# Kernel tuning notes

Measured on AMD Instinct MI355X. Metric: run time of the kernel, lower is better.

## Reference

```python
import jax, jax.numpy as jnp
import numpy as np

N_NODES = 50000
N_EDGES = 800000
F_IN = 2
T = 12
HID = 64
OUT = 12
K = 2  # diffusion order: identity + 1-hop (out- and in-directed)


def setup_inputs() -> dict:
    key = jax.random.key(0)
    ks = jax.random.split(key, 12)
    inp = {}
    inp["x"] = jax.random.normal(ks[0], (1, N_NODES, F_IN, T), dtype=jnp.float32)
    inp["edge_index"] = jax.random.randint(ks[1], (2, N_EDGES), 0, N_NODES)
    inp["edge_weight"] = jax.random.uniform(ks[2], (N_EDGES,), dtype=jnp.float32)

    def u(k, shape, fan):
        s = 1.0 / np.sqrt(fan)
        return jax.random.uniform(k, shape, jnp.float32, -s, s)

    c1 = F_IN + HID   # 66: DCRNN gates operate on cat([X, H])
    c2 = HID + HID    # 128
    inp["w1z"] = u(ks[3], (2, K, c1, HID), c1); inp["b1z"] = jnp.zeros((HID,), jnp.float32)
    inp["w1r"] = u(ks[4], (2, K, c1, HID), c1); inp["b1r"] = jnp.zeros((HID,), jnp.float32)
    inp["w1h"] = u(ks[5], (2, K, c1, HID), c1); inp["b1h"] = jnp.zeros((HID,), jnp.float32)
    inp["w2z"] = u(ks[6], (2, K, c2, HID), c2); inp["b2z"] = jnp.zeros((HID,), jnp.float32)
    inp["w2r"] = u(ks[7], (2, K, c2, HID), c2); inp["b2r"] = jnp.zeros((HID,), jnp.float32)
    inp["w2h"] = u(ks[8], (2, K, c2, HID), c2); inp["b2h"] = jnp.zeros((HID,), jnp.float32)
    inp["lin_w"] = u(ks[9], (HID, OUT), HID)
    inp["lin_b"] = u(ks[10], (OUT,), HID)
    return inp


def _dconv(X, row, col, norm_out, norm_in, w, b):
    # K=2 diffusion conv: H = X@W[:,0] + (D_O^-1 W diffusion)@W[0,1] + (D_I^-1 W^T diffusion)@W[1,1] + b
    H = X @ w[0, 0] + X @ w[1, 0]
    Xr = X[row]  # gather source-node features per edge: [E, C]
    Tx_o = jax.ops.segment_sum(norm_out[:, None] * Xr, col, num_segments=N_NODES)
    Tx_i = jax.ops.segment_sum(norm_in[:, None] * Xr, col, num_segments=N_NODES)
    return H + Tx_o @ w[0, 1] + Tx_i @ w[1, 1] + b


def _cell(X, H, row, col, no, ni, wz, bz, wr, br, wh, bh):
    # GRU-style DCRNN cell
    XH = jnp.concatenate([X, H], axis=1)
    Z = jax.nn.sigmoid(_dconv(XH, row, col, no, ni, wz, bz))
    R = jax.nn.sigmoid(_dconv(XH, row, col, no, ni, wr, br))
    Ht = jnp.tanh(_dconv(jnp.concatenate([X, R * H], axis=1), row, col, no, ni, wh, bh))
    return Z * H + (1.0 - Z) * Ht


def reference(x, edge_index, edge_weight, w1z, b1z, w1r, b1r, w1h, b1h,
              w2z, b2z, w2r, b2r, w2h, b2h, lin_w, lin_b):
    row, col = edge_index[0], edge_index[1]
    deg_out = jax.ops.segment_sum(edge_weight, row, num_segments=N_NODES)
    deg_in = jax.ops.segment_sum(edge_weight, col, num_segments=N_NODES)
    norm_out = edge_weight / deg_out[row]  # per-edge weight of D_O^{-1} W
    norm_in = edge_weight / deg_in[col]    # per-edge weight of D_I^{-1} W^T
    xs = jnp.transpose(x[0], (2, 0, 1))    # [T, N, F] (batch = 1)

    def step(carry, xt):
        h1, h2 = carry
        h1 = jax.nn.relu(_cell(xt, h1, row, col, norm_out, norm_in, w1z, b1z, w1r, b1r, w1h, b1h))
        h2 = jax.nn.relu(_cell(h1, h2, row, col, norm_out, norm_in, w2z, b2z, w2r, b2r, w2h, b2h))
        return (h1, h2), None

    h0 = jnp.zeros((N_NODES, HID), x.dtype)
    (h1, h2), _ = jax.lax.scan(step, (h0, h0), xs)
    out = h2 @ lin_w + lin_b  # [N, 12]
    return out.reshape(1, N_NODES, OUT)
```

## Files before the change

### kernel.cpp

```cpp
#include <hip/hip_runtime.h>

#define NN 50000
#define NE 800000
#define TT 12
#define NBIN (4 * NN)
#define NBLK ((NBIN + 255) / 256)

typedef _Float16 h16;
typedef __attribute__((ext_vector_type(2))) _Float16 h16x2;
typedef __attribute__((ext_vector_type(4))) _Float16 h16x4;
typedef __attribute__((ext_vector_type(8))) _Float16 half8;
typedef __attribute__((ext_vector_type(4))) float f32x4;
typedef __attribute__((address_space(3))) h16 as3h16;
typedef __attribute__((address_space(3))) half8 as3half8;

static constexpr size_t alignup(size_t x) { return (x + 255) & ~(size_t)255; }
static constexpr size_t O_CNT  = 0;
static constexpr size_t O_CUR  = alignup(O_CNT + NBIN + 1);
static constexpr size_t O_DEGO = alignup(O_CUR + NBIN);
static constexpr size_t O_BSUM = alignup(O_DEGO + NN);
static constexpr size_t O_BEXC = O_BSUM + 1024;
static constexpr size_t O_EDG  = alignup(O_BEXC + 1024);
static constexpr size_t O_TXX  = alignup(O_EDG + (size_t)NE * 2);
static constexpr size_t O_WF1ZR= alignup(O_TXX + (size_t)TT * NN * 4);
static constexpr size_t O_WF1H = alignup(O_WF1ZR + 12288);
static constexpr size_t O_WF2ZR= alignup(O_WF1H + 6144);
static constexpr size_t O_WF2H = alignup(O_WF2ZR + 24576);
static constexpr size_t O_WX1ZR= alignup(O_WF2H + 12288);
static constexpr size_t O_WX1H = alignup(O_WX1ZR + 768);
static constexpr size_t O_PX0  = alignup(O_WX1H + 384);
static constexpr size_t O_PX1  = O_PX0 + (size_t)NN * 64;
static constexpr size_t O_PZR  = O_PX1 + (size_t)NN * 64;
static constexpr size_t O_Z1   = O_PZR + (size_t)NN * 64;
static constexpr size_t O_Z2   = O_Z1 + (size_t)NN * 32;
static constexpr size_t O_TXA  = alignup(O_Z2 + (size_t)NN * 32);
static constexpr size_t O_TXB  = alignup(O_TXA + (size_t)NN * 64);
static constexpr size_t WS_FLOATS = O_TXB + (size_t)NN * 128;

__device__ __forceinline__ float sigm_(float x) { return 1.f / (1.f + __expf(-x)); }
__device__ __forceinline__ float tanh_(float x) { float e = __expf(2.f * x); return 1.f - 2.f / (e + 1.f); }

__device__ __forceinline__ void gld_lds16(const h16* g, as3h16* l) {
    __builtin_amdgcn_global_load_lds(
        (const __attribute__((address_space(1))) void*)g,
        (__attribute__((address_space(3))) void*)l, 16, 0, 0);
}

template <int N>
__device__ __forceinline__ void wait_lgkm0_vm() {
    if constexpr (N == 0)      asm volatile("s_waitcnt lgkmcnt(0) vmcnt(0)" ::: "memory");
    else if constexpr (N == 1) asm volatile("s_waitcnt lgkmcnt(0) vmcnt(1)" ::: "memory");
    else                       asm volatile("s_waitcnt lgkmcnt(0) vmcnt(2)" ::: "memory");
}


__global__ __launch_bounds__(256) void k_zero(float* ws) {
    size_t i = (size_t)blockIdx.x * 256 + threadIdx.x;
    size_t stride = (size_t)gridDim.x * 256;
    for (size_t p = i; p < O_BSUM + 2048; p += stride) ((int*)ws)[p] = 0;
    for (size_t p = i; p < (size_t)NN * 128; p += stride) ws[O_PX0 + p] = 0.f;
    for (size_t p = i; p < (size_t)NN * 128; p += stride) ws[O_TXB + p] = 0.f;
}

__global__ __launch_bounds__(256) void k_hist(const int* ei, float* ws) {
    int e = blockIdx.x * 256 + threadIdx.x;
    if (e >= NE) return;
    int r = ei[e], c = ei[NE + e];
    int bin = c * 4 + r / 12500;
    int rk = atomicAdd((int*)ws + O_CNT + bin, 1);
    ((int*)ws)[O_TXX + e] = rk;
}

__global__ __launch_bounds__(256) void k_scanA(float* ws) {
    __shared__ int sh[256];
    int t = threadIdx.x, i = blockIdx.x * 256 + t;
    int v = (i < NBIN) ? ((int*)ws)[O_CNT + i] : 0;
    sh[t] = v; __syncthreads();
    for (int o = 128; o > 0; o >>= 1) { if (t < o) sh[t] += sh[t + o]; __syncthreads(); }
    if (t == 0) ((int*)ws)[O_BSUM + blockIdx.x] = sh[0];
}

__global__ __launch_bounds__(256) void k_scanB(float* ws) {
    __shared__ int tot[256];
    int t = threadIdx.x;
    int* bsum = (int*)ws + O_BSUM;
    int* bexc = (int*)ws + O_BEXC;
    int base = t * 4;
    int v0 = (base + 0 < NBLK) ? bsum[base + 0] : 0;
    int v1 = (base + 1 < NBLK) ? bsum[base + 1] : 0;
    int v2 = (base + 2 < NBLK) ? bsum[base + 2] : 0;
    int v3 = (base + 3 < NBLK) ? bsum[base + 3] : 0;
    int sum = v0 + v1 + v2 + v3;
    tot[t] = sum; __syncthreads();
    for (int o = 1; o < 256; o <<= 1) {
        int a = (t >= o) ? tot[t - o] : 0;
        __syncthreads(); tot[t] += a; __syncthreads();
    }
    int excl = tot[t] - sum;
    if (base + 0 < NBLK) bexc[base + 0] = excl;
    if (base + 1 < NBLK) bexc[base + 1] = excl + v0;
    if (base + 2 < NBLK) bexc[base + 2] = excl + v0 + v1;
    if (base + 3 < NBLK) bexc[base + 3] = excl + v0 + v1 + v2;
    if (t == 255) ((int*)ws)[O_CNT + NBIN] = tot[255];
}

__global__ __launch_bounds__(256) void k_scanC(float* ws) {
    __shared__ int sh[256];
    int t = threadIdx.x, b = blockIdx.x, i = b * 256 + t;
    int v = (i < NBIN) ? ((int*)ws)[O_CNT + i] : 0;
    sh[t] = v; __syncthreads();
    for (int o = 1; o < 256; o <<= 1) {
        int a = (t >= o) ? sh[t - o] : 0;
        __syncthreads(); sh[t] += a; __syncthreads();
    }
    if (i < NBIN) ((int*)ws)[O_CNT + i] = ((int*)ws)[O_BEXC + b] + sh[t] - v;
}

__global__ __launch_bounds__(256) void k_scatter(const int* ei, const float* ew, float* ws) {
    int e = blockIdx.x * 256 + threadIdx.x;
    if (e >= NE) return;
    int r = ei[e], c = ei[NE + e];
    float w = ew[e];
    atomicAdd(ws + O_DEGO + r, w);
    int bin = c * 4 + r / 12500;
    int p = ((const int*)ws)[O_CNT + bin] + ((const int*)ws)[O_TXX + e];
    uint2 rec; rec.x = (unsigned)r; rec.y = __float_as_uint(w);
    ((uint2*)(ws + O_EDG))[p] = rec;
}

__global__ __launch_bounds__(256) void k_norm(float* ws) {
    int n = blockIdx.x * 4 + (threadIdx.x >> 6);
    int lane = threadIdx.x & 63;
    const int* offs = (const int*)ws + O_CNT;
    uint2* recs = (uint2*)(ws + O_EDG);
    const float* dego = ws + O_DEGO;
    int e0 = offs[4 * n], e1 = offs[4 * n + 4];
    float s = 0.f;
    for (int e = e0 + lane; e < e1; e += 64) s += __uint_as_float(recs[e].y);
    #pragma unroll
    for (int m = 1; m < 64; m <<= 1) s += __shfl_xor(s, m);
    float inv = 1.f / s;
    for (int e = e0 + lane; e < e1; e += 64) {
        uint2 r = recs[e];
        float w = __uint_as_float(r.y);
        h16x2 nv; nv.x = (h16)(w / dego[r.x]); nv.y = (h16)(w * inv);
        r.y = __builtin_bit_cast(unsigned int, nv);
        recs[e] = r;
    }
}

__global__ __launch_bounds__(256) void k_aggx(const float* __restrict__ x, float* __restrict__ ws) {
    int tid = threadIdx.x;
    int n = blockIdx.x * 8 + (tid >> 5);
    int l = tid & 31;
    const int* offs = (const int*)ws + O_CNT;
    const uint2* recs = (const uint2*)(ws + O_EDG);
    int e0 = offs[4 * n], e1 = offs[4 * n + 4];
    int f = l / 12, tt2 = l % 12;
    bool act = l < 24;
    float ao = 0.f, ai = 0.f;
    uint2 rc0, rc1;
    if (e0 < e1) {
        rc0 = recs[e0];
        rc1 = recs[(e0 + 1 < e1) ? e0 + 1 : e1 - 1];
    }
    for (int e = e0; e < e1; e += 2) {
        uint2 c0 = rc0, c1 = rc1;
        int n2 = (e + 2 < e1) ? e + 2 : e1 - 1, n3 = (e + 3 < e1) ? e + 3 : e1 - 1;
        rc0 = recs[n2]; rc1 = recs[n3];
        h16x2 nv0 = __builtin_bit_cast(h16x2, c0.y);
        h16x2 nv1 = __builtin_bit_cast(h16x2, c1.y);
        bool ok1 = (e + 1 < e1);
        float no1 = ok1 ? (float)nv1.x : 0.f, ni1 = ok1 ? (float)nv1.y : 0.f;
        if (act) {
            float v0 = x[(size_t)c0.x * 24 + f * 12 + tt2];
            float v1 = x[(size_t)c1.x * 24 + f * 12 + tt2];
            ao += (float)nv0.x * v0 + no1 * v1;
            ai += (float)nv0.y * v0 + ni1 * v1;
        }
    }
    if (act) {
        ws[O_TXX + ((size_t)tt2 * NN + n) * 4 + f] = ao;
        ws[O_TXX + ((size_t)tt2 * NN + n) * 4 + 2 + f] = ai;
    }
}

__device__ void packf_dev(int L, int NO, const float* wa, const float* wb, h16* Wf, int idx) {
    int C = (L == 1) ? 66 : 128;
    int NT = NO / 16;
    int j = idx & 7, l = (idx >> 3) & 63;
    int rest = idx >> 9;
    int ct = rest % NT, ks = rest / NT;
    int k = ks * 32 + ((l >> 4) << 3) + j;
    int col = ct * 16 + (l & 15);
    const float* w = wa; int jj = col;
    if (NO == 128 && col >= 64) { w = wb; jj = col - 64; }
    int G = k >> 6, c6 = k & 63, sg, crow;
    if (L == 1) { sg = G; crow = 2 + c6; }
    else        { sg = G >> 1; crow = ((G & 1) << 6) + c6; }
    float v;
    if (sg == 0)      v = w[(size_t)(0 * C + crow) * 64 + jj] + w[(size_t)(2 * C + crow) * 64 + jj];
    else if (sg == 1) v = w[(size_t)(1 * C + crow) * 64 + jj];
    else              v = w[(size_t)(3 * C + crow) * 64 + jj];
    Wf[idx] = (h16)v;
}

__device__ void packx_dev(int NO, const float* wa, const float* wb, float* Wx, int idx) {
    if (idx >= 6 * NO) return;
    int cc = idx / NO, col = idx % NO;
    const float* w = wa; int jj = col;
    if (NO == 128 && col >= 64) { w = wb; jj = col - 64; }
    int sg = cc >> 1, c = cc & 1;
    float v;
    if (sg == 0)      v = w[(size_t)(0 * 66 + c) * 64 + jj] + w[(size_t)(2 * 66 + c) * 64 + jj];
    else if (sg == 1) v = w[(size_t)(1 * 66 + c) * 64 + jj];
    else              v = w[(size_t)(3 * 66 + c) * 64 + jj];
    Wx[idx] = v;
}

__global__ __launch_bounds__(256) void k_packall(const float* w1z, const float* w1r, const float* w1h,
    const float* w2z, const float* w2r, const float* w2h, float* ws) {
    int b = blockIdx.x, t = threadIdx.x;
    if (b < 96)       packf_dev(1, 128, w1z, w1r, (h16*)(ws + O_WF1ZR), b * 256 + t);
    else if (b < 144) packf_dev(1, 64,  w1h, nullptr, (h16*)(ws + O_WF1H), (b - 96) * 256 + t);
    else if (b < 336) packf_dev(2, 128, w2z, w2r, (h16*)(ws + O_WF2ZR), (b - 144) * 256 + t);
    else if (b < 432) packf_dev(2, 64,  w2h, nullptr, (h16*)(ws + O_WF2H), (b - 336) * 256 + t);
    else {
        int idx = (b - 432) * 256 + t;
        if (idx < 768) packx_dev(128, w1z, w1r, ws + O_WX1ZR, idx);
        int idx2 = idx - 768;
        if (idx2 >= 0 && idx2 < 384) packx_dev(64, w1h, nullptr, ws + O_WX1H, idx2);
    }
}

__global__ __launch_bounds__(256) void k_aggP(
    const h16* __restrict__ T,
    h16* __restrict__ outA, int orsA, int oA, int iA,
    h16* __restrict__ outB, int orsB, int oB, int iB,
    const float* __restrict__ ws) {
    int tid = threadIdx.x, lane = tid & 63, wv = tid >> 6;
    int q = lane >> 4, fl = lane & 15;
    int n = blockIdx.x * 16 + wv * 4 + q;
    const int* offs = (const int*)ws + O_CNT;
    const uint2* recs = (const uint2*)(ws + O_EDG);
    int e0 = offs[4 * n], e1 = offs[4 * n + 4];
    float ao[8] = {}, ai[8] = {};
    for (int e = e0; e < e1; e += 4) {
        int i1 = e + 1 < e1 ? e + 1 : e1 - 1;
        int i2 = e + 2 < e1 ? e + 2 : e1 - 1;
        int i3 = e + 3 < e1 ? e + 3 : e1 - 1;
        uint2 r0 = recs[e], r1 = recs[i1], r2 = recs[i2], r3 = recs[i3];
        half8 v0 = *(const half8*)(T + (size_t)r0.x * 128 + fl * 8);
        half8 v1 = *(const half8*)(T + (size_t)r1.x * 128 + fl * 8);
        half8 v2 = *(const half8*)(T + (size_t)r2.x * 128 + fl * 8);
        half8 v3 = *(const half8*)(T + (size_t)r3.x * 128 + fl * 8);
        h16x2 m0 = __builtin_bit_cast(h16x2, r0.y);
        h16x2 m1 = __builtin_bit_cast(h16x2, r1.y);
        h16x2 m2 = __builtin_bit_cast(h16x2, r2.y);
        h16x2 m3 = __builtin_bit_cast(h16x2, r3.y);
        float no0 = (float)m0.x, ni0 = (float)m0.y;
        float no1 = (e + 1 < e1) ? (float)m1.x : 0.f, ni1 = (e + 1 < e1) ? (float)m1.y : 0.f;
        float no2 = (e + 2 < e1) ? (float)m2.x : 0.f, ni2 = (e + 2 < e1) ? (float)m2.y : 0.f;
        float no3 = (e + 3 < e1) ? (float)m3.x : 0.f, ni3 = (e + 3 < e1) ? (float)m3.y : 0.f;
        #pragma unroll
        for (int j = 0; j < 8; ++j) {
            float f0 = (float)v0[j], f1 = (float)v1[j], f2 = (float)v2[j], f3 = (float)v3[j];
            ao[j] += no0 * f0 + no1 * f1 + no2 * f2 + no3 * f3;
            ai[j] += ni0 * f0 + ni1 * f1 + ni2 * f2 + ni3 * f3;
        }
    }
    h16* outP = (fl < 8) ? outA : outB;
    int ors = (fl < 8) ? orsA : orsB;
    int fo = (fl < 8) ? fl : fl - 8;
    int oT = ((fl < 8) ? oA : oB) + fo * 8;
    int iT = ((fl < 8) ? iA : iB) + fo * 8;
    half8 wo, wi;
    #pragma unroll
    for (int j = 0; j < 8; ++j) { wo[j] = (h16)ao[j]; wi[j] = (h16)ai[j]; }
    *(half8*)(outP + (size_t)n * ors + oT) = wo;
    *(half8*)(outP + (size_t)n * ors + iT) = wi;
}

__global__ __launch_bounds__(256) void k_agg1(
    const h16* __restrict__ T, int hs,
    h16* __restrict__ out, int ors, int oA, int iA,
    const float* __restrict__ ws) {
    int tid = threadIdx.x, lane = tid & 63, wv = tid >> 6;
    int q = lane >> 3, fl = lane & 7;
    int n = blockIdx.x * 32 + wv * 8 + q;
    if (n >= NN) n = NN - 1;
    const int* offs = (const int*)ws + O_CNT;
    const uint2* recs = (const uint2*)(ws + O_EDG);
    int e0 = offs[4 * n], e1 = offs[4 * n + 4];
    float ao[8] = {}, ai[8] = {};
    for (int e = e0; e < e1; e += 2) {
        int i1 = e + 1 < e1 ? e + 1 : e1 - 1;
        uint2 r0 = recs[e], r1 = recs[i1];
        half8 v0 = *(const half8*)(T + (size_t)r0.x * hs + fl * 8);
        half8 v1 = *(const half8*)(T + (size_t)r1.x * hs + fl * 8);
        h16x2 m0 = __builtin_bit_cast(h16x2, r0.y);
        h16x2 m1 = __builtin_bit_cast(h16x2, r1.y);
        float no0 = (float)m0.x, ni0 = (float)m0.y;
        float no1 = (e + 1 < e1) ? (float)m1.x : 0.f, ni1 = (e + 1 < e1) ? (float)m1.y : 0.f;
        #pragma unroll
        for (int j = 0; j < 8; ++j) {
            float f0 = (float)v0[j], f1 = (float)v1[j];
            ao[j] += no0 * f0 + no1 * f1;
            ai[j] += ni0 * f0 + ni1 * f1;
        }
    }
    half8 wo, wi;
    #pragma unroll
    for (int j = 0; j < 8; ++j) { wo[j] = (h16)ao[j]; wi[j] = (h16)ai[j]; }
    *(half8*)(out + (size_t)n * ors + oA + fl * 8) = wo;
    *(half8*)(out + (size_t)n * ors + iA + fl * 8) = wi;
}

struct Seg { const h16* p[6]; int st[6]; int of[6]; };
#define RB ((NN + 63) / 64)

template <int G>
__device__ __forceinline__ void stage_g(as3h16* lds, const Seg& seg, int bi, int lane, int rh, int cq) {
    int r16 = lane & 15, kg = lane >> 4;
    int gr0 = bi * 64 + cq * 16 + r16; if (gr0 >= NN) gr0 = NN - 1;
    gld_lds16(seg.p[G] + (size_t)gr0 * seg.st[G] + seg.of[G] + rh * 32 + kg * 8,
              lds + (G & 3) * 4096 + (rh * 4 + cq) * 512);
}

template <int G, int NG, int CT>
__device__ __forceinline__ void gsteps(as3h16* lds, const Seg& seg, int bi, int lane, int rh, int cq,
                                       half8 (&wreg)[NG * 2][CT], f32x4 (&acc)[2][CT]) {
    if constexpr (G < NG) {
        constexpr int OUT = (NG - 1 - G) >= 2 ? 2 : (NG - 1 - G);
        wait_lgkm0_vm<OUT>();
        __builtin_amdgcn_s_barrier();
        asm volatile("" ::: "memory");
        if constexpr (G + 3 < NG) stage_g<G + 3>(lds, seg, bi, lane, rh, cq);
        #pragma unroll
        for (int kk = 0; kk < 2; ++kk) {
            half8 af[2];
            #pragma unroll
            for (int s = 0; s < 2; ++s)
                af[s] = *(const as3half8*)(lds + (G & 3) * 4096 + (kk * 4 + rh * 2 + s) * 512 + lane * 8);
            #pragma unroll
            for (int c = 0; c < CT; ++c)
                #pragma unroll
                for (int s = 0; s < 2; ++s)
                    acc[s][c] = __builtin_amdgcn_mfma_f32_16x16x32_f16(af[s], wreg[2 * G + kk][c], acc[s][c], 0, 0, 0);
        }
        gsteps<G + 1, NG, CT>(lds, seg, bi, lane, rh, cq, wreg, acc);
    }
}

template <int NG, int NO, int CT, int EPI, int XEPI>
__device__ __forceinline__ void mmg_body(int bi, const Seg& seg, const h16* __restrict__ Wf,
    const float* __restrict__ Wx, const float* __restrict__ x, const float* __restrict__ txx, int t,
    const float* __restrict__ Ba, const float* __restrict__ Bb,
    const h16* Hprev, h16* zbuf, h16* rhh, h16* houth, as3h16* lds) {
    constexpr int KS = NG * 2;
    constexpr int NT = NO / 16;
    int tid = threadIdx.x, lane = tid & 63, wv = tid >> 6;
    int cq = wv & 3, rh = wv >> 2;
    int ctb = cq * CT;
    int r16 = lane & 15;

    half8 wreg[KS][CT];
    #pragma unroll
    for (int ks = 0; ks < KS; ++ks)
        #pragma unroll
        for (int c = 0; c < CT; ++c)
            wreg[ks][c] = *(const half8*)(Wf + (((size_t)ks * NT + ctb + c) * 64 + lane) * 8);

    stage_g<0>(lds, seg, bi, lane, rh, cq);
    stage_g<1>(lds, seg, bi, lane, rh, cq);
    stage_g<2>(lds, seg, bi, lane, rh, cq);

    f32x4 acc[2][CT];
    #pragma unroll
    for (int s = 0; s < 2; ++s)
        #pragma unroll
        for (int c = 0; c < CT; ++c) acc[s][c] = (f32x4){0.f, 0.f, 0.f, 0.f};

    gsteps<0, NG, CT>(lds, seg, bi, lane, rh, cq, wreg, acc);

    int row0 = bi * 64 + rh * 32;
    int rg4 = (lane >> 4) * 4;
    #pragma unroll
    for (int s = 0; s < 2; ++s) {
        int rbase = row0 + s * 16 + rg4;
        float xa0[4], xa1[4]; float4 tg[4];
        if (XEPI) {
            #pragma unroll
            for (int r = 0; r < 4; ++r) {
                int row = rbase + r; if (row >= NN) row = NN - 1;
                xa0[r] = x[(size_t)row * 24 + t];
                xa1[r] = x[(size_t)row * 24 + 12 + t];
                tg[r] = *(const float4*)&txx[((size_t)t * NN + row) * 4];
            }
        }
        #pragma unroll
        for (int c = 0; c < CT; ++c) {
            int col = (ctb + c) * 16 + r16;
            float w0, w1, w2, w3, w4, w5;
            if (XEPI) {
                w0 = Wx[col]; w1 = Wx[NO + col]; w2 = Wx[2 * NO + col];
                w3 = Wx[3 * NO + col]; w4 = Wx[4 * NO + col]; w5 = Wx[5 * NO + col];
            }
            float bb = (EPI == 0) ? (col < 64 ? Ba[col] : Bb[col - 64]) : Ba[col];
            #pragma unroll
            for (int r = 0; r < 4; ++r) {
                int row = rbase + r;
                if (row >= NN) continue;
                float v = acc[s][c][r] + bb;
                if (XEPI) v += xa0[r] * w0 + xa1[r] * w1 + tg[r].x * w2 + tg[r].y * w3 + tg[r].z * w4 + tg[r].w * w5;
                if (EPI == 0) {
                    if (col < 64) zbuf[(size_t)row * 64 + col] = (h16)sigm_(v);
                    else {
                        float rr_ = sigm_(v);
                        float hp = (float)Hprev[(size_t)row * 128 + col - 64];
                        rhh[(size_t)row * 128 + col - 64] = (h16)(rr_ * hp);
                    }
                } else {
                    float ht = tanh_(v);
                    float z = (float)zbuf[(size_t)row * 64 + col];
                    float hp = (float)Hprev[(size_t)row * 128 + col];
                    float hn = fmaxf(z * hp + (1.f - z) * ht, 0.f);
                    houth[(size_t)row * 128 + col] = (h16)hn;
                }
            }
        }
    }
}

template <int NG, int NO, int CT, int EPI, int XEPI>
__global__ __launch_bounds__(512, 2) void k_mmg(Seg seg, const h16* __restrict__ Wf,
    const float* __restrict__ Wx, const float* __restrict__ x, const float* __restrict__ txx, int t,
    const float* __restrict__ Ba, const float* __restrict__ Bb,
    const h16* Hprev, h16* zbuf, h16* rhh, h16* houth) {
    __shared__ __align__(16) h16 smem[4 * 4096];
    mmg_body<NG, NO, CT, EPI, XEPI>(blockIdx.x, seg, Wf, Wx, x, txx, t, Ba, Bb, Hprev, zbuf, rhh, houth,
                                    (as3h16*)smem);
}

__global__ __launch_bounds__(512, 2) void k_mmzr2(Seg sA, Seg sB,
    const h16* __restrict__ wfA, const h16* __restrict__ wfB, const float* __restrict__ wxB,
    const float* __restrict__ x, const float* __restrict__ txx, int tB,
    const float* __restrict__ bAz, const float* __restrict__ bAr,
    const float* __restrict__ bBz, const float* __restrict__ bBr,
    const h16* hpA, h16* zA, h16* rhA,
    const h16* hpB, h16* zB, h16* rhB) {
    __shared__ __align__(16) h16 smem[4 * 4096];
    if (blockIdx.x < RB)
        mmg_body<6, 128, 2, 0, 0>(blockIdx.x, sA, wfA, nullptr, nullptr, nullptr, 0, bAz, bAr,
                                  hpA, zA, rhA, nullptr, (as3h16*)smem);
    else
        mmg_body<3, 128, 2, 0, 1>(blockIdx.x - RB, sB, wfB, wxB, x, txx, tB, bBz, bBr,
                                  hpB, zB, rhB, nullptr, (as3h16*)smem);
}

__global__ __launch_bounds__(512, 2) void k_mmh2(Seg sA, Seg sB,
    const h16* __restrict__ wfA, const h16* __restrict__ wfB, const float* __restrict__ wxB,
    const float* __restrict__ x, const float* __restrict__ txx, int tB,
    const float* __restrict__ bAh, const float* __restrict__ bBh,
    h16* zA, const h16* hpA, h16* hoA,
    h16* zB, const h16* hpB, h16* hoB) {
    __shared__ __align__(16) h16 smem[4 * 4096];
    if (blockIdx.x < RB)
        mmg_body<6, 64, 1, 1, 0>(blockIdx.x, sA, wfA, nullptr, nullptr, nullptr, 0, bAh, nullptr,
                                 hpA, zA, nullptr, hoA, (as3h16*)smem);
    else
        mmg_body<3, 64, 1, 1, 1>(blockIdx.x - RB, sB, wfB, wxB, x, txx, tB, bBh, nullptr,
                                 hpB, zB, nullptr, hoB, (as3h16*)smem);
}

__global__ __launch_bounds__(256) void k_final(const h16* __restrict__ h2p, const float* __restrict__ lw,
                                               const float* __restrict__ lb, float* __restrict__ out) {
    __shared__ float sh[16 * 65];
    int t = threadIdx.x;
    int n0 = blockIdx.x * 16;
    int idx = t * 4;
    int nl = idx >> 6, h = idx & 63;
    h16x4 v = *(const h16x4*)&h2p[(size_t)(n0 + nl) * 128 + h];
    sh[nl * 65 + h] = (float)v[0]; sh[nl * 65 + h + 1] = (float)v[1];
    sh[nl * 65 + h + 2] = (float)v[2]; sh[nl * 65 + h + 3] = (float)v[3];
    __syncthreads();
    if (t < 192) {
        int n = t / 12, o = t % 12;
        float acc = lb[o];
        #pragma unroll 8
        for (int k = 0; k < 64; ++k) acc += sh[n * 65 + k] * lw[k * 12 + o];
        out[(size_t)(n0 + n) * 12 + o] = acc;
    }
}

extern "C" void kernel_launch(void* const* d_in, const int* in_sizes, int n_in,
                              void* d_out, int out_size, void* d_ws, size_t ws_size,
                              hipStream_t stream) {
    const float* x   = (const float*)d_in[0];
    const int*   ei  = (const int*)d_in[1];
    const float* ew  = (const float*)d_in[2];
    const float* w1z = (const float*)d_in[3];  const float* b1z = (const float*)d_in[4];
    const float* w1r = (const float*)d_in[5];  const float* b1r = (const float*)d_in[6];
    const float* w1h = (const float*)d_in[7];  const float* b1h = (const float*)d_in[8];
    const float* w2z = (const float*)d_in[9];  const float* b2z = (const float*)d_in[10];
    const float* w2r = (const float*)d_in[11]; const float* b2r = (const float*)d_in[12];
    const float* w2h = (const float*)d_in[13]; const float* b2h = (const float*)d_in[14];
    const float* lw  = (const float*)d_in[15]; const float* lb  = (const float*)d_in[16];
    float* out = (float*)d_out;
    float* ws  = (float*)d_ws;
    if (ws_size < WS_FLOATS * sizeof(float)) return;

    k_zero<<<2048, 256, 0, stream>>>(ws);
    k_hist<<<(NE + 255) / 256, 256, 0, stream>>>(ei, ws);
    k_scanA<<<NBLK, 256, 0, stream>>>(ws);
    k_scanB<<<1, 256, 0, stream>>>(ws);
    k_scanC<<<NBLK, 256, 0, stream>>>(ws);
    k_scatter<<<(NE + 255) / 256, 256, 0, stream>>>(ei, ew, ws);
    k_norm<<<NN / 4, 256, 0, stream>>>(ws);
    k_aggx<<<NN / 8, 256, 0, stream>>>(x, ws);
    k_packall<<<437, 256, 0, stream>>>(w1z, w1r, w1h, w2z, w2r, w2h, ws);

    h16* pEven = (h16*)(ws + O_PX0);
    h16* pOdd  = (h16*)(ws + O_PX1);
    h16* pzr   = (h16*)(ws + O_PZR);
    h16* z1    = (h16*)(ws + O_Z1);
    h16* z2    = (h16*)(ws + O_Z2);
    h16* txA = (h16*)(ws + O_TXA);
    h16* txB = (h16*)(ws + O_TXB);
    const float* txx = ws + O_TXX;
    const h16* wf1zr = (const h16*)(ws + O_WF1ZR);
    const h16* wf1h  = (const h16*)(ws + O_WF1H);
    const h16* wf2zr = (const h16*)(ws + O_WF2ZR);
    const h16* wf2h  = (const h16*)(ws + O_WF2H);
    const float* wx1zr = ws + O_WX1ZR;
    const float* wx1h  = ws + O_WX1H;
    const int GAP = NN / 16;
    const int GA1 = (NN + 31) / 32;

    auto s1zr = [&](h16* px) -> Seg {
        return {{px, txB, txB, nullptr, nullptr, nullptr}, {128, 256, 256, 0, 0, 0}, {0, 0, 128, 0, 0, 0}};
    };
    Seg s1h = {{pzr, txA, txA, nullptr, nullptr, nullptr}, {128, 128, 128, 0, 0, 0}, {0, 0, 64, 0, 0, 0}};
    auto s2zr = [&](h16* px) -> Seg {
        return {{px, px, txB, txB, txB, txB}, {128, 128, 256, 256, 256, 256}, {0, 64, 0, 64, 128, 192}};
    };
    auto s2h = [&](h16* px) -> Seg {
        return {{px, pzr, txB, txB, txB, txB}, {128, 128, 256, 256, 256, 256}, {0, 64, 0, 64, 128, 192}};
    };

    k_mmg<3, 128, 2, 0, 1><<<RB, 512, 0, stream>>>(s1zr(pOdd), wf1zr, wx1zr, x, txx, 0,
        b1z, b1r, pOdd, z1, pzr, nullptr);
    k_agg1<<<GA1, 256, 0, stream>>>(pzr, 128, txA, 128, 0, 64, ws);
    k_mmg<3, 64, 1, 1, 1><<<RB, 512, 0, stream>>>(s1h, wf1h, wx1h, x, txx, 0,
        b1h, nullptr, pOdd, z1, nullptr, pEven);
    k_aggP<<<GAP, 256, 0, stream>>>(pEven, txB, 256, 0, 128, txB, 256, 64, 192, ws);

    for (int t = 0; t < TT - 1; ++t) {
        h16* pxT  = (t & 1) ? pOdd : pEven;
        h16* pxT1 = (t & 1) ? pEven : pOdd;
        k_mmzr2<<<RB * 2, 512, 0, stream>>>(s2zr(pxT), s1zr(pxT), wf2zr, wf1zr, wx1zr,
            x, txx, t + 1, b2z, b2r, b1z, b1r,
            pxT + 64, z2, pzr + 64,
            pxT,      z1, pzr);
        k_aggP<<<GAP, 256, 0, stream>>>(pzr, txA, 128, 0, 64, txB, 256, 64, 192, ws);
        k_mmh2<<<RB * 2, 512, 0, stream>>>(s2h(pxT), s1h, wf2h, wf1h, wx1h,
            x, txx, t + 1, b2h, b1h,
            z2, pxT + 64, pxT1 + 64,
            z1, pxT,      pxT1);
        k_aggP<<<GAP, 256, 0, stream>>>(pxT1, txB, 256, 0, 128, txB, 256, 64, 192, ws);
    }

    k_mmg<6, 128, 2, 0, 0><<<RB, 512, 0, stream>>>(s2zr(pOdd), wf2zr, nullptr, nullptr, nullptr, 0,
        b2z, b2r, pOdd + 64, z2, pzr + 64, nullptr);
    k_agg1<<<GA1, 256, 0, stream>>>(pzr + 64, 128, txB, 256, 64, 192, ws);
    k_mmg<6, 64, 1, 1, 0><<<RB, 512, 0, stream>>>(s2h(pOdd), wf2h, nullptr, nullptr, nullptr, 0,
        b2h, nullptr, pOdd + 64, z2, nullptr, pEven + 64);
    k_final<<<NN / 16, 256, 0, stream>>>(pEven + 64, lw, lb, out);
}
```

Baseline: 1.695 ms.

## Prefetch edge records in aggregation loops and process two row tiles per GEMM block

```diff
diff --git a/kernel.cpp b/kernel.cpp
--- a/kernel.cpp
+++ b/kernel.cpp
@@ -245,19 +245,29 @@
     const uint2* recs = (const uint2*)(ws + O_EDG);
     int e0 = offs[4 * n], e1 = offs[4 * n + 4];
     float ao[8] = {}, ai[8] = {};
+    uint2 pr0, pr1, pr2, pr3;
+    if (e0 < e1) {
+        int i1 = e0 + 1 < e1 ? e0 + 1 : e1 - 1;
+        int i2 = e0 + 2 < e1 ? e0 + 2 : e1 - 1;
+        int i3 = e0 + 3 < e1 ? e0 + 3 : e1 - 1;
+        pr0 = recs[e0]; pr1 = recs[i1]; pr2 = recs[i2]; pr3 = recs[i3];
+    }
     for (int e = e0; e < e1; e += 4) {
-        int i1 = e + 1 < e1 ? e + 1 : e1 - 1;
-        int i2 = e + 2 < e1 ? e + 2 : e1 - 1;
-        int i3 = e + 3 < e1 ? e + 3 : e1 - 1;
-        uint2 r0 = recs[e], r1 = recs[i1], r2 = recs[i2], r3 = recs[i3];
-        half8 v0 = *(const half8*)(T + (size_t)r0.x * 128 + fl * 8);
-        half8 v1 = *(const half8*)(T + (size_t)r1.x * 128 + fl * 8);
-        half8 v2 = *(const half8*)(T + (size_t)r2.x * 128 + fl * 8);
-        half8 v3 = *(const half8*)(T + (size_t)r3.x * 128 + fl * 8);
-        h16x2 m0 = __builtin_bit_cast(h16x2, r0.y);
-        h16x2 m1 = __builtin_bit_cast(h16x2, r1.y);
-        h16x2 m2 = __builtin_bit_cast(h16x2, r2.y);
-        h16x2 m3 = __builtin_bit_cast(h16x2, r3.y);
+        uint2 c0 = pr0, c1 = pr1, c2 = pr2, c3 = pr3;
+        int ne = e + 4;
+        int j0 = ne < e1 ? ne : e1 - 1;
+        int j1 = ne + 1 < e1 ? ne + 1 : e1 - 1;
+        int j2 = ne + 2 < e1 ? ne + 2 : e1 - 1;
+        int j3 = ne + 3 < e1 ? ne + 3 : e1 - 1;
+        pr0 = recs[j0]; pr1 = recs[j1]; pr2 = recs[j2]; pr3 = recs[j3];
+        half8 v0 = *(const half8*)(T + (size_t)c0.x * 128 + fl * 8);
+        half8 v1 = *(const half8*)(T + (size_t)c1.x * 128 + fl * 8);
+        half8 v2 = *(const half8*)(T + (size_t)c2.x * 128 + fl * 8);
+        half8 v3 = *(const half8*)(T + (size_t)c3.x * 128 + fl * 8);
+        h16x2 m0 = __builtin_bit_cast(h16x2, c0.y);
+        h16x2 m1 = __builtin_bit_cast(h16x2, c1.y);
+        h16x2 m2 = __builtin_bit_cast(h16x2, c2.y);
+        h16x2 m3 = __builtin_bit_cast(h16x2, c3.y);
         float no0 = (float)m0.x, ni0 = (float)m0.y;
         float no1 = (e + 1 < e1) ? (float)m1.x : 0.f, ni1 = (e + 1 < e1) ? (float)m1.y : 0.f;
         float no2 = (e + 2 < e1) ? (float)m2.x : 0.f, ni2 = (e + 2 < e1) ? (float)m2.y : 0.f;
@@ -293,13 +303,21 @@
     const uint2* recs = (const uint2*)(ws + O_EDG);
     int e0 = offs[4 * n], e1 = offs[4 * n + 4];
     float ao[8] = {}, ai[8] = {};
+    uint2 pr0, pr1;
+    if (e0 < e1) {
+        pr0 = recs[e0];
+        pr1 = recs[(e0 + 1 < e1) ? e0 + 1 : e1 - 1];
+    }
     for (int e = e0; e < e1; e += 2) {
-        int i1 = e + 1 < e1 ? e + 1 : e1 - 1;
-        uint2 r0 = recs[e], r1 = recs[i1];
-        half8 v0 = *(const half8*)(T + (size_t)r0.x * hs + fl * 8);
-        half8 v1 = *(const half8*)(T + (size_t)r1.x * hs + fl * 8);
-        h16x2 m0 = __builtin_bit_cast(h16x2, r0.y);
-        h16x2 m1 = __builtin_bit_cast(h16x2, r1.y);
+        uint2 c0 = pr0, c1 = pr1;
+        int ne = e + 2;
+        int j0 = ne < e1 ? ne : e1 - 1;
+        int j1 = ne + 1 < e1 ? ne + 1 : e1 - 1;
+        pr0 = recs[j0]; pr1 = recs[j1];
+        half8 v0 = *(const half8*)(T + (size_t)c0.x * hs + fl * 8);
+        half8 v1 = *(const half8*)(T + (size_t)c1.x * hs + fl * 8);
+        h16x2 m0 = __builtin_bit_cast(h16x2, c0.y);
+        h16x2 m1 = __builtin_bit_cast(h16x2, c1.y);
         float no0 = (float)m0.x, ni0 = (float)m0.y;
         float no1 = (e + 1 < e1) ? (float)m1.x : 0.f, ni1 = (e + 1 < e1) ? (float)m1.y : 0.f;
         #pragma unroll
@@ -318,6 +336,8 @@
 
 struct Seg { const h16* p[6]; int st[6]; int of[6]; };
 #define RB ((NN + 63) / 64)
+#define RBT ((RB + 1) / 2)
+#define TPB 2
 
 template <int G>
 __device__ __forceinline__ void stage_g(as3h16* lds, const Seg& seg, int bi, int lane, int rh, int cq) {
@@ -353,7 +373,7 @@
 }
 
 template <int NG, int NO, int CT, int EPI, int XEPI>
-__device__ __forceinline__ void mmg_body(int bi, const Seg& seg, const h16* __restrict__ Wf,
+__device__ __forceinline__ void mmg_body(int pb, const Seg& seg, const h16* __restrict__ Wf,
     const float* __restrict__ Wx, const float* __restrict__ x, const float* __restrict__ txx, int t,
     const float* __restrict__ Ba, const float* __restrict__ Bb,
     const h16* Hprev, h16* zbuf, h16* rhh, h16* houth, as3h16* lds) {
@@ -363,6 +383,7 @@
     int cq = wv & 3, rh = wv >> 2;
     int ctb = cq * CT;
     int r16 = lane & 15;
+    int rg4 = (lane >> 4) * 4;
 
     half8 wreg[KS][CT];
     #pragma unroll
@@ -371,63 +392,75 @@
         for (int c = 0; c < CT; ++c)
             wreg[ks][c] = *(const half8*)(Wf + (((size_t)ks * NT + ctb + c) * 64 + lane) * 8);
 
-    stage_g<0>(lds, seg, bi, lane, rh, cq);
-    stage_g<1>(lds, seg, bi, lane, rh, cq);
-    stage_g<2>(lds, seg, bi, lane, rh, cq);
-
-    f32x4 acc[2][CT];
     #pragma unroll
-    for (int s = 0; s < 2; ++s)
+    for (int ti = 0; ti < TPB; ++ti) {
+        int bi = pb * TPB + ti;
+        if (ti == 0) {
+            stage_g<0>(lds, seg, bi, lane, rh, cq);
+            stage_g<1>(lds, seg, bi, lane, rh, cq);
+            stage_g<2>(lds, seg, bi, lane, rh, cq);
+        }
+
+        f32x4 acc[2][CT];
         #pragma unroll
-        for (int c = 0; c < CT; ++c) acc[s][c] = (f32x4){0.f, 0.f, 0.f, 0.f};
-
-    gsteps<0, NG, CT>(lds, seg, bi, lane, rh, cq, wreg, acc);
-
-    int row0 = bi * 64 + rh * 32;
-    int rg4 = (lane >> 4) * 4;
-    #pragma unroll
-    for (int s = 0; s < 2; ++s) {
-        int rbase = row0 + s * 16 + rg4;
-        float xa0[4], xa1[4]; float4 tg[4];
-        if (XEPI) {
+        for (int s = 0; s < 2; ++s)
             #pragma unroll
-            for (int r = 0; r < 4; ++r) {
-                int row = rbase + r; if (row >= NN) row = NN - 1;
-                xa0[r] = x[(size_t)row * 24 + t];
-                xa1[r] = x[(size_t)row * 24 + 12 + t];
-                tg[r] = *(const float4*)&txx[((size_t)t * NN + row) * 4];
+            for (int c = 0; c < CT; ++c) acc[s][c] = (f32x4){0.f, 0.f, 0.f, 0.f};
+
+        gsteps<0, NG, CT>(lds, seg, bi, lane, rh, cq, wreg, acc);
+
+        int row0 = bi * 64 + rh * 32;
+        #pragma unroll
+        for (int s = 0; s < 2; ++s) {
+            int rbase = row0 + s * 16 + rg4;
+            float xa0[4], xa1[4]; float4 tg[4];
+            if (XEPI) {
+                #pragma unroll
+                for (int r = 0; r < 4; ++r) {
+                    int row = rbase + r; if (row >= NN) row = NN - 1;
+                    xa0[r] = x[(size_t)row * 24 + t];
+                    xa1[r] = x[(size_t)row * 24 + 12 + t];
+                    tg[r] = *(const float4*)&txx[((size_t)t * NN + row) * 4];
+                }
+            }
+            #pragma unroll
+            for (int c = 0; c < CT; ++c) {
+                int col = (ctb + c) * 16 + r16;
+                float w0, w1, w2, w3, w4, w5;
+                if (XEPI) {
+                    w0 = Wx[col]; w1 = Wx[NO + col]; w2 = Wx[2 * NO + col];
+                    w3 = Wx[3 * NO + col]; w4 = Wx[4 * NO + col]; w5 = Wx[5 * NO + col];
+                }
+                float bb = (EPI == 0) ? (col < 64 ? Ba[col] : Bb[col - 64]) : Ba[col];
+                #pragma unroll
+                for (int r = 0; r < 4; ++r) {
+                    int row = rbase + r;
+                    if (row >= NN) continue;
+                    float v = acc[s][c][r] + bb;
+                    if (XEPI) v += xa0[r] * w0 + xa1[r] * w1 + tg[r].x * w2 + tg[r].y * w3 + tg[r].z * w4 + tg[r].w * w5;
+                    if (EPI == 0) {
+                        if (col < 64) zbuf[(size_t)row * 64 + col] = (h16)sigm_(v);
+                        else {
+                            float rr_ = sigm_(v);
+                            float hp = (float)Hprev[(size_t)row * 128 + col - 64];
+                            rhh[(size_t)row * 128 + col - 64] = (h16)(rr_ * hp);
+                        }
+                    } else {
+                        float ht = tanh_(v);
+                        float z = (float)zbuf[(size_t)row * 64 + col];
+                        float hp = (float)Hprev[(size_t)row * 128 + col];
+                        float hn = fmaxf(z * hp + (1.f - z) * ht, 0.f);
+                        houth[(size_t)row * 128 + col] = (h16)hn;
+                    }
+                }
             }
         }
-        #pragma unroll
-        for (int c = 0; c < CT; ++c) {
-            int col = (ctb + c) * 16 + r16;
-            float w0, w1, w2, w3, w4, w5;
-            if (XEPI) {
-                w0 = Wx[col]; w1 = Wx[NO + col]; w2 = Wx[2 * NO + col];
-                w3 = Wx[3 * NO + col]; w4 = Wx[4 * NO + col]; w5 = Wx[5 * NO + col];
-            }
-            float bb = (EPI == 0) ? (col < 64 ? Ba[col] : Bb[col - 64]) : Ba[col];
-            #pragma unroll
-            for (int r = 0; r < 4; ++r) {
-                int row = rbase + r;
-                if (row >= NN) continue;
-                float v = acc[s][c][r] + bb;
-                if (XEPI) v += xa0[r] * w0 + xa1[r] * w1 + tg[r].x * w2 + tg[r].y * w3 + tg[r].z * w4 + tg[r].w * w5;
-                if (EPI == 0) {
-                    if (col < 64) zbuf[(size_t)row * 64 + col] = (h16)sigm_(v);
-                    else {
-                        float rr_ = sigm_(v);
-                        float hp = (float)Hprev[(size_t)row * 128 + col - 64];
-                        rhh[(size_t)row * 128 + col - 64] = (h16)(rr_ * hp);
-                    }
-                } else {
-                    float ht = tanh_(v);
-                    float z = (float)zbuf[(size_t)row * 64 + col];
-                    float hp = (float)Hprev[(size_t)row * 128 + col];
-                    float hn = fmaxf(z * hp + (1.f - z) * ht, 0.f);
-                    houth[(size_t)row * 128 + col] = (h16)hn;
-                }
-            }
+
+        if (ti + 1 < TPB) {
+            __syncthreads();
+            stage_g<0>(lds, seg, bi + 1, lane, rh, cq);
+            stage_g<1>(lds, seg, bi + 1, lane, rh, cq);
+            stage_g<2>(lds, seg, bi + 1, lane, rh, cq);
         }
     }
 }
@@ -450,11 +483,11 @@
     const h16* hpA, h16* zA, h16* rhA,
     const h16* hpB, h16* zB, h16* rhB) {
     __shared__ __align__(16) h16 smem[4 * 4096];
-    if (blockIdx.x < RB)
+    if (blockIdx.x < RBT)
         mmg_body<6, 128, 2, 0, 0>(blockIdx.x, sA, wfA, nullptr, nullptr, nullptr, 0, bAz, bAr,
                                   hpA, zA, rhA, nullptr, (as3h16*)smem);
     else
-        mmg_body<3, 128, 2, 0, 1>(blockIdx.x - RB, sB, wfB, wxB, x, txx, tB, bBz, bBr,
+        mmg_body<3, 128, 2, 0, 1>(blockIdx.x - RBT, sB, wfB, wxB, x, txx, tB, bBz, bBr,
                                   hpB, zB, rhB, nullptr, (as3h16*)smem);
 }
 
@@ -465,11 +498,11 @@
     h16* zA, const h16* hpA, h16* hoA,
     h16* zB, const h16* hpB, h16* hoB) {
     __shared__ __align__(16) h16 smem[4 * 4096];
-    if (blockIdx.x < RB)
+    if (blockIdx.x < RBT)
         mmg_body<6, 64, 1, 1, 0>(blockIdx.x, sA, wfA, nullptr, nullptr, nullptr, 0, bAh, nullptr,
                                  hpA, zA, nullptr, hoA, (as3h16*)smem);
     else
-        mmg_body<3, 64, 1, 1, 1>(blockIdx.x - RB, sB, wfB, wxB, x, txx, tB, bBh, nullptr,
+        mmg_body<3, 64, 1, 1, 1>(blockIdx.x - RBT, sB, wfB, wxB, x, txx, tB, bBh, nullptr,
                                  hpB, zB, nullptr, hoB, (as3h16*)smem);
 }
 
@@ -548,32 +581,32 @@
         return {{px, pzr, txB, txB, txB, txB}, {128, 128, 256, 256, 256, 256}, {0, 64, 0, 64, 128, 192}};
     };
 
-    k_mmg<3, 128, 2, 0, 1><<<RB, 512, 0, stream>>>(s1zr(pOdd), wf1zr, wx1zr, x, txx, 0,
+    k_mmg<3, 128, 2, 0, 1><<<RBT, 512, 0, stream>>>(s1zr(pOdd), wf1zr, wx1zr, x, txx, 0,
         b1z, b1r, pOdd, z1, pzr, nullptr);
     k_agg1<<<GA1, 256, 0, stream>>>(pzr, 128, txA, 128, 0, 64, ws);
-    k_mmg<3, 64, 1, 1, 1><<<RB, 512, 0, stream>>>(s1h, wf1h, wx1h, x, txx, 0,
+    k_mmg<3, 64, 1, 1, 1><<<RBT, 512, 0, stream>>>(s1h, wf1h, wx1h, x, txx, 0,
         b1h, nullptr, pOdd, z1, nullptr, pEven);
     k_aggP<<<GAP, 256, 0, stream>>>(pEven, txB, 256, 0, 128, txB, 256, 64, 192, ws);
 
     for (int t = 0; t < TT - 1; ++t) {
         h16* pxT  = (t & 1) ? pOdd : pEven;
         h16* pxT1 = (t & 1) ? pEven : pOdd;
-        k_mmzr2<<<RB * 2, 512, 0, stream>>>(s2zr(pxT), s1zr(pxT), wf2zr, wf1zr, wx1zr,
+        k_mmzr2<<<RBT * 2, 512, 0, stream>>>(s2zr(pxT), s1zr(pxT), wf2zr, wf1zr, wx1zr,
             x, txx, t + 1, b2z, b2r, b1z, b1r,
             pxT + 64, z2, pzr + 64,
             pxT,      z1, pzr);
         k_aggP<<<GAP, 256, 0, stream>>>(pzr, txA, 128, 0, 64, txB, 256, 64, 192, ws);
-        k_mmh2<<<RB * 2, 512, 0, stream>>>(s2h(pxT), s1h, wf2h, wf1h, wx1h,
+        k_mmh2<<<RBT * 2, 512, 0, stream>>>(s2h(pxT), s1h, wf2h, wf1h, wx1h,
             x, txx, t + 1, b2h, b1h,
             z2, pxT + 64, pxT1 + 64,
             z1, pxT,      pxT1);
         k_aggP<<<GAP, 256, 0, stream>>>(pxT1, txB, 256, 0, 128, txB, 256, 64, 192, ws);
     }
 
-    k_mmg<6, 128, 2, 0, 0><<<RB, 512, 0, stream>>>(s2zr(pOdd), wf2zr, nullptr, nullptr, nullptr, 0,
+    k_mmg<6, 128, 2, 0, 0><<<RBT, 512, 0, stream>>>(s2zr(pOdd), wf2zr, nullptr, nullptr, nullptr, 0,
         b2z, b2r, pOdd + 64, z2, pzr + 64, nullptr);
     k_agg1<<<GA1, 256, 0, stream>>>(pzr + 64, 128, txB, 256, 64, 192, ws);
-    k_mmg<6, 64, 1, 1, 0><<<RB, 512, 0, stream>>>(s2h(pOdd), wf2h, nullptr, nullptr, nullptr, 0,
+    k_mmg<6, 64, 1, 1, 0><<<RBT, 512, 0, stream>>>(s2h(pOdd), wf2h, nullptr, nullptr, nullptr, 0,
         b2h, nullptr, pOdd + 64, z2, nullptr, pEven + 64);
     k_final<<<NN / 16, 256, 0, stream>>>(pEven + 64, lw, lb, out);
 }
```

After: 1.976 ms. 16.6% more time.
